# Optimization experiments

Measured on AMD Instinct MI355X. Metric: run time of the kernel, lower is better.

The kernel has to match this reference:

```python
import jax, jax.numpy as jnp
import numpy as np

B, T, HOR, N = 64, 12, 12, 1024
DIN, DOUT, YCOV, H, K, E = 1, 1, 1, 64, 3, 8


def setup_inputs() -> dict:
    key = jax.random.key(0)
    ks = jax.random.split(key, 10)
    def g(k, shape, s=1.0):
        return jax.random.normal(k, shape, dtype=jnp.float32) * s
    # xavier-ish scale for GCN weights: 1/sqrt(fan_in)
    gi = 1.0 / np.sqrt(K * (DIN + H))
    di = 1.0 / np.sqrt(K * (DOUT + YCOV + H))
    return {
        "x": jax.random.uniform(ks[0], (B, T, N, DIN), dtype=jnp.float32),
        "y_cov": jax.random.uniform(ks[1], (B, HOR, N, YCOV), dtype=jnp.float32),
        "node_emb": g(ks[2], (N, E), 1.0),
        "enc_gate_W": g(ks[3], (K * (DIN + H), 2 * H), gi),
        "enc_gate_b": jnp.zeros((2 * H,), jnp.float32),
        "enc_upd_W": g(ks[4], (K * (DIN + H), H), gi),
        "enc_upd_b": jnp.zeros((H,), jnp.float32),
        "dec_gate_W": g(ks[5], (K * (DOUT + YCOV + H), 2 * H), di),
        "dec_gate_b": jnp.zeros((2 * H,), jnp.float32),
        "dec_upd_W": g(ks[6], (K * (DOUT + YCOV + H), H), di),
        "dec_upd_b": jnp.zeros((H,), jnp.float32),
        "proj_W": g(ks[7], (H, DOUT), 1.0 / np.sqrt(H)),
        "proj_b": jnp.zeros((DOUT,), jnp.float32),
    }


def _cheb_supports(A):
    # support_set = [I, A, 2*A@A - I, ...], cheb_k terms
    s = [jnp.eye(A.shape[0], dtype=A.dtype), A]
    for _ in range(2, K):
        s.append(2.0 * A @ s[-1] - s[-2])
    return jnp.stack(s)  # [K, N, N]


def _gcn(x, sup, W, b):
    # x: [B,N,C]; sup: [K,N,N]; matches torch cat([s_k @ x], -1) ordering (k-major)
    bb, nn, cc = x.shape
    xg = jnp.einsum('knm,bmc->bnkc', sup, x).reshape(bb, nn, K * cc)
    return xg @ W + b


def _cell(x, h, sup, gW, gb, uW, ub):
    zr = jax.nn.sigmoid(_gcn(jnp.concatenate([x, h], -1), sup, gW, gb))
    z, r = jnp.split(zr, 2, axis=-1)
    hc = jnp.tanh(_gcn(jnp.concatenate([x, z * h], -1), sup, uW, ub))
    return r * h + (1.0 - r) * hc


def reference(x, y_cov, node_emb, enc_gate_W, enc_gate_b, enc_upd_W, enc_upd_b,
              dec_gate_W, dec_gate_b, dec_upd_W, dec_upd_b, proj_W, proj_b):
    # adaptive adjacency from node embeddings (AGCRN-style)
    A = jax.nn.softmax(jax.nn.relu(node_emb @ node_emb.T), axis=-1)
    sup = _cheb_supports(A)

    h0 = jnp.zeros((B, N, H), x.dtype)

    def enc_step(h, xt):
        h2 = _cell(xt, h, sup, enc_gate_W, enc_gate_b, enc_upd_W, enc_upd_b)
        return h2, None
    h_enc, _ = jax.lax.scan(enc_step, h0, jnp.swapaxes(x, 0, 1))  # final state [B,N,H]

    go0 = jnp.zeros((B, N, DOUT), x.dtype)

    def dec_step(carry, yt):
        h, go = carry
        h2 = _cell(jnp.concatenate([go, yt], -1), h, sup,
                   dec_gate_W, dec_gate_b, dec_upd_W, dec_upd_b)
        go2 = h2 @ proj_W + proj_b
        return (h2, go2), go2
    _, outs = jax.lax.scan(dec_step, (h_enc, go0), jnp.swapaxes(y_cov, 0, 1))
    return jnp.swapaxes(outs, 0, 1)  # [B, HOR, N, DOUT]
```

## Files before the change

kernel.cpp:

```cpp
#include <hip/hip_runtime.h>
#include <math.h>

constexpr int N = 1024, B = 64, T = 12, HOR = 12, H = 64, E = 8;
constexpr size_t NBH = 4194304;

constexpr size_t A_off   = 0;
constexpr size_t Pxy_off = 1048576;
constexpr size_t h_off   = Pxy_off + 3145728;
constexpr size_t Ph_off  = h_off + NBH;
constexpr size_t zh_off  = Ph_off + 2 * NBH;
constexpr size_t r_off   = zh_off + NBH;
constexpr size_t go_off  = r_off + NBH;
constexpr size_t A2_off  = go_off + 65536;
constexpr size_t Bth_off = A2_off + 1048576;
constexpr size_t Btz_off = Bth_off + 2162688;
constexpr size_t xyK_off = Btz_off + 2097152;
constexpr size_t Pgo_off = xyK_off + 786432;
constexpr size_t wp_off  = Pgo_off + 131072;

typedef __attribute__((ext_vector_type(8))) short short8;
typedef __attribute__((ext_vector_type(4))) float f32x4;

__device__ __forceinline__ unsigned f2bf(float x) {
  unsigned u = __float_as_uint(x);
  return (u + 0x7fffu + ((u >> 16) & 1u)) >> 16;
}
__device__ __forceinline__ float bf2f(unsigned h) {
  return __uint_as_float(h << 16);
}
__device__ __forceinline__ void split4(float4 v, uint2& hi, uint2& lo) {
  unsigned h0 = f2bf(v.x), h1 = f2bf(v.y), h2 = f2bf(v.z), h3 = f2bf(v.w);
  unsigned l0 = f2bf(v.x - bf2f(h0)), l1 = f2bf(v.y - bf2f(h1));
  unsigned l2 = f2bf(v.z - bf2f(h2)), l3 = f2bf(v.w - bf2f(h3));
  hi.x = (h0 & 0xffffu) | (h1 << 16); hi.y = (h2 & 0xffffu) | (h3 << 16);
  lo.x = (l0 & 0xffffu) | (l1 << 16); lo.y = (l2 & 0xffffu) | (l3 << 16);
}

typedef const __attribute__((address_space(1))) void gas_t;
typedef __attribute__((address_space(3))) void las_t;

__global__ __launch_bounds__(256) void build_A(const float* __restrict__ emb,
                                               float* __restrict__ A) {
  __shared__ float sE[N * E];
  __shared__ float sv[N];
  __shared__ float rmax[4], rsum[4];
  const int i = blockIdx.x;
  for (int idx = threadIdx.x; idx < N * E / 4; idx += 256)
    ((float4*)sE)[idx] = ((const float4*)emb)[idx];
  __syncthreads();
  float ei[E];
#pragma unroll
  for (int e = 0; e < E; ++e) ei[e] = sE[i * E + e];
  float mymax = 0.f;
  for (int j = threadIdx.x; j < N; j += 256) {
    float d = 0.f;
#pragma unroll
    for (int e = 0; e < E; ++e) d = fmaf(ei[e], sE[j * E + e], d);
    d = fmaxf(d, 0.f);
    sv[j] = d;
    mymax = fmaxf(mymax, d);
  }
  for (int off = 32; off; off >>= 1) mymax = fmaxf(mymax, __shfl_down(mymax, off));
  const int wid = threadIdx.x >> 6, lid = threadIdx.x & 63;
  if (lid == 0) rmax[wid] = mymax;
  __syncthreads();
  const float m = fmaxf(fmaxf(rmax[0], rmax[1]), fmaxf(rmax[2], rmax[3]));
  float mysum = 0.f;
  for (int j = threadIdx.x; j < N; j += 256) {
    float ev = expf(sv[j] - m);
    sv[j] = ev;
    mysum += ev;
  }
  for (int off = 32; off; off >>= 1) mysum += __shfl_down(mysum, off);
  if (lid == 0) rsum[wid] = mysum;
  __syncthreads();
  const float inv = 1.f / (rsum[0] + rsum[1] + rsum[2] + rsum[3]);
  for (int j = threadIdx.x; j < N; j += 256) A[i * N + j] = sv[j] * inv;
}

__global__ __launch_bounds__(256) void pack_split_S(const float* __restrict__ A,
                                                    ushort* __restrict__ L,
                                                    ushort* __restrict__ R) {
  __shared__ float tile[32][33];
  const int bx = blockIdx.x * 32;
  const int by = blockIdx.y * 32;
  const int tx = threadIdx.x & 31;
  const int tg = threadIdx.x >> 5;
#pragma unroll
  for (int p = 0; p < 4; ++p) {
    int ty = tg * 4 + p;
    tile[ty][tx] = A[(size_t)(by + ty) * 1024 + bx + tx];
  }
  __syncthreads();
#pragma unroll
  for (int p = 0; p < 4; ++p) {
    int ty = tg * 4 + p;
    float v = tile[ty][tx];
    unsigned h = f2bf(v);
    unsigned l = f2bf(v - bf2f(h));
    size_t lb = (size_t)(by + ty) * 3072 + 3 * (bx + tx);
    L[lb + 0] = (ushort)h; L[lb + 1] = (ushort)l; L[lb + 2] = (ushort)h;
    float w = tile[tx][ty];
    unsigned hh = f2bf(w);
    unsigned ll = f2bf(w - bf2f(hh));
    size_t rbi = (size_t)(bx + ty) * 3072 + 3 * (by + tx);
    R[rbi + 0] = (ushort)hh; R[rbi + 1] = (ushort)hh; R[rbi + 2] = (ushort)ll;
  }
}

__global__ __launch_bounds__(256) void conv_bf16(const float* __restrict__ src,
                                                 ushort* __restrict__ dst) {
  int i = blockIdx.x * 256 + threadIdx.x;
  float4 v = ((const float4*)src)[i];
  ushort4 o;
  o.x = (ushort)f2bf(v.x); o.y = (ushort)f2bf(v.y);
  o.z = (ushort)f2bf(v.z); o.w = (ushort)f2bf(v.w);
  ((ushort4*)dst)[i] = o;
}

__global__ __launch_bounds__(256) void conv_xyK(const float* __restrict__ src,
                                                ushort* __restrict__ dst, int off) {
  int id = blockIdx.x * 256 + threadIdx.x;
  int tb = id >> 10, n = id & 1023;
  int tt = tb >> 6, b = tb & 63;
  dst[(size_t)(off + tb) * 1024 + n] = (ushort)f2bf(src[((size_t)b * T + tt) * 1024 + n]);
}

__global__ __launch_bounds__(256) void pack_W(const float* __restrict__ W,
                                              ushort* __restrict__ out,
                                              int CIN, int NC, int xoff) {
  int idx = blockIdx.x * 256 + threadIdx.x;
  int total = 3 * 2 * NC * 32;
  if (idx >= total) return;
  int kk = idx & 31;
  int colrest = idx >> 5;
  int col = colrest % NC;
  int rest = colrest / NC;
  int half = rest & 1;
  int s = rest >> 1;
  float v = W[(size_t)(s * CIN + xoff + half * 32 + kk) * NC + col];
  unsigned hi = f2bf(v);
  unsigned lo = f2bf(v - bf2f(hi));
  size_t base = (size_t)((s * 2 + half) * 2) * NC * 32;
  out[base + (size_t)col * 32 + kk] = (ushort)hi;
  out[base + (size_t)NC * 32 + (size_t)col * 32 + kk] = (ushort)lo;
}

__global__ __launch_bounds__(256) void gemm_s2p(
    const ushort* __restrict__ L, const ushort* __restrict__ R,
    float* __restrict__ P) {
  __shared__ ushort As[128 * 32];
  __shared__ ushort Bs[128 * 32];
  const int t = threadIdx.x;
  const int wave = t >> 6, lane = t & 63;
  const int bm = blockIdx.y * 128, bn = blockIdx.x * 128;
  const int wm = (wave & 1) * 64, wn = (wave >> 1) * 64;
  float* Pz = P + (size_t)blockIdx.z * 1048576;
  const int kbase = blockIdx.z * 768;

  const ushort* aSrc[2]; const ushort* bSrc[2];
  ushort* aDst[2]; ushort* bDst[2];
#pragma unroll
  for (int u = 0; u < 2; ++u) {
    int idx = wave * 128 + u * 64 + lane;
    int row = idx >> 2;
    int kq = (idx & 3) * 8;
    aSrc[u] = L + (size_t)(bm + row) * 3072 + kq;
    bSrc[u] = R + (size_t)(bn + row) * 3072 + kq;
    aDst[u] = &As[(wave * 128 + u * 64) * 8];
    bDst[u] = &Bs[(wave * 128 + u * 64) * 8];
  }
  const int lr = lane & 15;
  const int lk = (lane >> 4) * 8;
  f32x4 acc[4][4];
#pragma unroll
  for (int i = 0; i < 4; ++i)
#pragma unroll
    for (int j = 0; j < 4; ++j) acc[i][j] = {0.f, 0.f, 0.f, 0.f};

  for (int k0 = kbase; k0 < kbase + 768; k0 += 32) {
#pragma unroll
    for (int u = 0; u < 2; ++u) {
      __builtin_amdgcn_global_load_lds((gas_t*)(aSrc[u] + k0), (las_t*)aDst[u], 16, 0, 0);
      __builtin_amdgcn_global_load_lds((gas_t*)(bSrc[u] + k0), (las_t*)bDst[u], 16, 0, 0);
    }
    __syncthreads();
    short8 a[4], b[4];
#pragma unroll
    for (int i = 0; i < 4; ++i) a[i] = *(const short8*)&As[(wm + i * 16 + lr) * 32 + lk];
#pragma unroll
    for (int j = 0; j < 4; ++j) b[j] = *(const short8*)&Bs[(wn + j * 16 + lr) * 32 + lk];
#pragma unroll
    for (int i = 0; i < 4; ++i)
#pragma unroll
      for (int j = 0; j < 4; ++j)
        acc[i][j] = __builtin_amdgcn_mfma_f32_16x16x32_bf16(a[i], b[j], acc[i][j], 0, 0, 0);
    __syncthreads();
  }
  const int cr = (lane >> 4) * 4;
  const int cc = lane & 15;
#pragma unroll
  for (int i = 0; i < 4; ++i)
#pragma unroll
    for (int j = 0; j < 4; ++j) {
      int gm = bm + wm + i * 16 + cr;
      int gn = bn + wn + j * 16 + cc;
#pragma unroll
      for (int r = 0; r < 4; ++r)
        Pz[(size_t)(gm + r) * 1024 + gn] = acc[i][j][r];
    }
}

__global__ __launch_bounds__(256) void comb_s2(const float* __restrict__ P,
                                               ushort* __restrict__ A2) {
  int idx = blockIdx.x * 256 + threadIdx.x;
  float4 a = ((const float4*)P)[idx];
  float4 b = ((const float4*)(P + 1048576))[idx];
  float4 c = ((const float4*)(P + 2097152))[idx];
  float4 d = ((const float4*)(P + 3145728))[idx];
  int base = idx << 2;
  int m = base >> 10, c0 = base & 1023;
  float v0 = 2.f * (a.x + b.x + c.x + d.x) - (m == c0 + 0 ? 1.f : 0.f);
  float v1 = 2.f * (a.y + b.y + c.y + d.y) - (m == c0 + 1 ? 1.f : 0.f);
  float v2 = 2.f * (a.z + b.z + c.z + d.z) - (m == c0 + 2 ? 1.f : 0.f);
  float v3 = 2.f * (a.w + b.w + c.w + d.w) - (m == c0 + 3 ? 1.f : 0.f);
  ushort4 o;
  o.x = (ushort)f2bf(v0); o.y = (ushort)f2bf(v1);
  o.z = (ushort)f2bf(v2); o.w = (ushort)f2bf(v3);
  ((ushort4*)(A2 + 1048576))[idx] = o;
}

template <int CMODE>
__global__ __launch_bounds__(256) void gemm_bt(
    const ushort* __restrict__ A2, const ushort* __restrict__ Bt, int n1,
    float* __restrict__ C1, float* __restrict__ C2) {
  __shared__ ushort As[2][128 * 32];
  __shared__ ushort Bs[2][128 * 32];
  const int t = threadIdx.x;
  const int wave = t >> 6, lane = t & 63;
  const int bm = blockIdx.y * 128, bn = blockIdx.x * 128;
  const int wm = (wave & 1) * 64, wn = (wave >> 1) * 64;

  const ushort* aSrc[2]; const ushort* bSrc[2];
  ushort* aDst[2][2]; ushort* bDst[2][2];
#pragma unroll
  for (int u = 0; u < 2; ++u) {
    int idx = wave * 128 + u * 64 + lane;
    int row = idx >> 2;
    int kq = (idx & 3) * 8;
    aSrc[u] = A2 + (size_t)(bm + row) * 1024 + kq;
    bSrc[u] = Bt + (size_t)(bn + row) * 1024 + kq;
#pragma unroll
    for (int p = 0; p < 2; ++p) {
      aDst[p][u] = &As[p][(wave * 128 + u * 64) * 8];
      bDst[p][u] = &Bs[p][(wave * 128 + u * 64) * 8];
    }
  }
  const int lr = lane & 15, lk = (lane >> 4) * 8;
  int aOff[4], bOff[4];
#pragma unroll
  for (int i = 0; i < 4; ++i) {
    aOff[i] = (wm + i * 16 + lr) * 32 + lk;
    bOff[i] = (wn + i * 16 + lr) * 32 + lk;
  }
  f32x4 acc[4][4];
#pragma unroll
  for (int i = 0; i < 4; ++i)
#pragma unroll
    for (int j = 0; j < 4; ++j) acc[i][j] = {0.f, 0.f, 0.f, 0.f};

  for (int k0 = 0; k0 < 1024; k0 += 64) {
#pragma unroll
    for (int p = 0; p < 2; ++p)
#pragma unroll
      for (int u = 0; u < 2; ++u) {
        __builtin_amdgcn_global_load_lds((gas_t*)(aSrc[u] + k0 + p * 32),
                                         (las_t*)aDst[p][u], 16, 0, 0);
        __builtin_amdgcn_global_load_lds((gas_t*)(bSrc[u] + k0 + p * 32),
                                         (las_t*)bDst[p][u], 16, 0, 0);
      }
    __syncthreads();
#pragma unroll
    for (int p = 0; p < 2; ++p) {
      short8 a[4], b[4];
#pragma unroll
      for (int i = 0; i < 4; ++i) a[i] = *(const short8*)&As[p][aOff[i]];
#pragma unroll
      for (int j = 0; j < 4; ++j) b[j] = *(const short8*)&Bs[p][bOff[j]];
#pragma unroll
      for (int i = 0; i < 4; ++i)
#pragma unroll
        for (int j = 0; j < 4; ++j)
          acc[i][j] = __builtin_amdgcn_mfma_f32_16x16x32_bf16(a[i], b[j], acc[i][j], 0, 0, 0);
    }
    __syncthreads();
  }

  const int cr = (lane >> 4) * 4;
  const int cc = lane & 15;
#pragma unroll
  for (int i = 0; i < 4; ++i) {
#pragma unroll
    for (int j = 0; j < 4; ++j) {
      int gm = bm + wm + i * 16 + cr;
      int gn = bn + wn + j * 16 + cc;
      if (gn < n1) {
        if (CMODE == 0) {
          float* p = C1 + (size_t)gm * n1 + gn;
#pragma unroll
          for (int r = 0; r < 4; ++r) p[(size_t)r * n1] = acc[i][j][r];
        } else {
          int half = gm >> 10, nn = gm & 1023;
          float* p = C1 + (size_t)half * NBH +
                     ((size_t)(gn >> 6) * 1024 + nn) * 64 + (gn & 63);
#pragma unroll
          for (int r = 0; r < 4; ++r) p[(size_t)r * 64] = acc[i][j][r];
        }
      } else if (C2 != nullptr && gn < n1 + 64) {
        float* p = C2 + (size_t)gm * 64 + (gn - n1);
#pragma unroll
        for (int r = 0; r < 4; ++r) p[(size_t)r * 64] = acc[i][j][r];
      }
    }
  }
}

template <int NX>
__global__ __launch_bounds__(256) void gate_mfma(
    const float* __restrict__ hmat, const float* __restrict__ Ph,
    const ushort* __restrict__ Wp, const float* __restrict__ Wf, const float* __restrict__ bias,
    const float* __restrict__ xb0, int xbs0, const float* __restrict__ xp0, int xs0,
    const float* __restrict__ xb1, int xbs1, const float* __restrict__ xp1, int xs1,
    float* __restrict__ zh, float* __restrict__ rbuf, ushort* __restrict__ Btz) {
  constexpr int CIN = NX + 64;
  __shared__ ushort Ah[128 * 32], Al[128 * 32];
  __shared__ ushort Bh[128 * 32], Bl[128 * 32];
  __shared__ ushort transT[64 * 136];
  __shared__ float sxv[3][2][128];
  __shared__ float sWx[3][2][128];
  const int t = threadIdx.x;
  const int wave = t >> 6, lane = t & 63;
  const int bm = blockIdx.x * 128;
  const int wm = (wave & 1) * 64, wn = (wave >> 1) * 64;
  const int lr = lane & 15, lk = (lane >> 4) * 8;
  const float* s1 = Ph;
  const float* s2 = Ph + NBH;

  if (t < 128) {
    int grow = bm + t;
    int n = grow & 1023, b = grow >> 10;
    sxv[0][0][t] = xb0[(size_t)b * xbs0 + n];
    sxv[1][0][t] = xp0[(size_t)n * xs0 + b];
    sxv[2][0][t] = xp0[(size_t)1024 * xs0 + (size_t)n * xs0 + b];
    if (NX == 2) {
      sxv[0][1][t] = xb1[(size_t)b * xbs1 + n];
      sxv[1][1][t] = xp1[(size_t)n * xs1 + b];
      sxv[2][1][t] = xp1[(size_t)1024 * xs1 + (size_t)n * xs1 + b];
    }
  } else {
    int col = t - 128;
#pragma unroll
    for (int s = 0; s < 3; ++s)
#pragma unroll
      for (int f = 0; f < NX; ++f)
        sWx[s][f][col] = Wf[(size_t)(s * CIN + f) * 128 + col];
  }

  f32x4 acc[4][4];
#pragma unroll
  for (int i = 0; i < 4; ++i)
#pragma unroll
    for (int j = 0; j < 4; ++j) acc[i][j] = {0.f, 0.f, 0.f, 0.f};

  for (int it = 0; it < 6; ++it) {
    const int s = it >> 1, half = it & 1, j0 = half * 32;
    const float* src = (s == 0) ? hmat : ((s == 1) ? s1 : s2);
#pragma unroll
    for (int p = 0; p < 4; ++p) {
      int f = p * 256 + t;
      int row = f >> 3;
      int jq = (f & 7) * 4;
      float4 v = *(const float4*)(src + (size_t)(bm + row) * 64 + j0 + jq);
      uint2 hi, lo;
      split4(v, hi, lo);
      *(uint2*)&Ah[row * 32 + jq] = hi;
      *(uint2*)&Al[row * 32 + jq] = lo;
    }
    const ushort* wph = Wp + (size_t)((s * 2 + half) * 2) * (128 * 32);
    const ushort* wpl = wph + 128 * 32;
#pragma unroll
    for (int u = 0; u < 2; ++u) {
      int idx = wave * 128 + u * 64 + lane;
      __builtin_amdgcn_global_load_lds((gas_t*)(wph + idx * 8), (las_t*)&Bh[idx * 8], 16, 0, 0);
      __builtin_amdgcn_global_load_lds((gas_t*)(wpl + idx * 8), (las_t*)&Bl[idx * 8], 16, 0, 0);
    }
    __syncthreads();
    short8 ah[4], al[4], bh[4], bl[4];
#pragma unroll
    for (int i = 0; i < 4; ++i) {
      ah[i] = *(const short8*)&Ah[(wm + i * 16 + lr) * 32 + lk];
      al[i] = *(const short8*)&Al[(wm + i * 16 + lr) * 32 + lk];
    }
#pragma unroll
    for (int j = 0; j < 4; ++j) {
      bh[j] = *(const short8*)&Bh[(wn + j * 16 + lr) * 32 + lk];
      bl[j] = *(const short8*)&Bl[(wn + j * 16 + lr) * 32 + lk];
    }
#pragma unroll
    for (int i = 0; i < 4; ++i)
#pragma unroll
      for (int j = 0; j < 4; ++j) {
        acc[i][j] = __builtin_amdgcn_mfma_f32_16x16x32_bf16(ah[i], bh[j], acc[i][j], 0, 0, 0);
        acc[i][j] = __builtin_amdgcn_mfma_f32_16x16x32_bf16(al[i], bh[j], acc[i][j], 0, 0, 0);
        acc[i][j] = __builtin_amdgcn_mfma_f32_16x16x32_bf16(ah[i], bl[j], acc[i][j], 0, 0, 0);
      }
    __syncthreads();
  }

  const int cr = (lane >> 4) * 4;
  const int cc = lane & 15;
#pragma unroll
  for (int i = 0; i < 4; ++i) {
#pragma unroll
    for (int j = 0; j < 4; ++j) {
      int col = wn + j * 16 + cc;
      float bcol = bias[col];
#pragma unroll
      for (int r = 0; r < 4; ++r) {
        int rowl = wm + i * 16 + cr + r;
        int grow = bm + rowl;
        float v = acc[i][j][r] + bcol;
#pragma unroll
        for (int s = 0; s < 3; ++s)
#pragma unroll
          for (int f = 0; f < NX; ++f)
            v = fmaf(sxv[s][f][rowl], sWx[s][f][col], v);
        float sig = 1.f / (1.f + expf(-v));
        if (col < 64) {
          float zv = sig * hmat[(size_t)grow * 64 + col];
          zh[(size_t)grow * 64 + col] = zv;
          transT[col * 136 + rowl] = (ushort)f2bf(zv);
        } else {
          rbuf[(size_t)grow * 64 + col - 64] = sig;
        }
      }
    }
  }
  __syncthreads();
  const int bq = bm >> 10, nb = bm & 1023;
  for (int idx = t; idx < 1024; idx += 256) {
    int j = idx >> 4, ch = idx & 15;
    uint4 v = *(const uint4*)&transT[j * 136 + ch * 8];
    *(uint4*)(Btz + (((size_t)(bq * 64 + j)) << 10) + nb + ch * 8) = v;
  }
}

template <int NX, int PROJ>
__global__ __launch_bounds__(256) void upd_mfma(
    float* __restrict__ hmat, const float* __restrict__ zhb, const float* __restrict__ Pzh,
    const ushort* __restrict__ Wp, const float* __restrict__ Wf, const float* __restrict__ bias,
    const float* __restrict__ xb0, int xbs0, const float* __restrict__ xp0, int xs0,
    const float* __restrict__ xb1, int xbs1, const float* __restrict__ xp1, int xs1,
    const float* __restrict__ rbuf, ushort* __restrict__ Bth,
    const float* __restrict__ pW, const float* __restrict__ pb,
    float* __restrict__ gobuf, float* __restrict__ outp, int tstep) {
  constexpr int CIN = NX + 64;
  __shared__ ushort Ah[128 * 32], Al[128 * 32];
  __shared__ ushort Bh[64 * 32], Bl[64 * 32];
  __shared__ ushort transT[64 * 136];
  __shared__ float sxv[3][2][128];
  __shared__ float sWx[3][2][64];
  __shared__ float part[2][128];
  const int t = threadIdx.x;
  const int wave = t >> 6, lane = t & 63;
  const int bm = blockIdx.x * 128;
  const int wm = (wave & 1) * 64, wn = (wave >> 1) * 32;
  const int lr = lane & 15, lk = (lane >> 4) * 8;
  const float* s1 = Pzh;
  const float* s2 = Pzh + NBH;

  if (t < 128) {
    int grow = bm + t;
    int n = grow & 1023, b = grow >> 10;
    sxv[0][0][t] = xb0[(size_t)b * xbs0 + n];
    sxv[1][0][t] = xp0[(size_t)n * xs0 + b];
    sxv[2][0][t] = xp0[(size_t)1024 * xs0 + (size_t)n * xs0 + b];
    if (NX == 2) {
      sxv[0][1][t] = xb1[(size_t)b * xbs1 + n];
      sxv[1][1][t] = xp1[(size_t)n * xs1 + b];
      sxv[2][1][t] = xp1[(size_t)1024 * xs1 + (size_t)n * xs1 + b];
    }
  } else if (t < 192) {
    int col = t - 128;
#pragma unroll
    for (int s = 0; s < 3; ++s)
#pragma unroll
      for (int f = 0; f < NX; ++f)
        sWx[s][f][col] = Wf[(size_t)(s * CIN + f) * 64 + col];
  }

  f32x4 acc[4][2];
#pragma unroll
  for (int i = 0; i < 4; ++i)
#pragma unroll
    for (int j = 0; j < 2; ++j) acc[i][j] = {0.f, 0.f, 0.f, 0.f};

  for (int it = 0; it < 6; ++it) {
    const int s = it >> 1, half = it & 1, j0 = half * 32;
    const float* src = (s == 0) ? zhb : ((s == 1) ? s1 : s2);
#pragma unroll
    for (int p = 0; p < 4; ++p) {
      int f = p * 256 + t;
      int row = f >> 3;
      int jq = (f & 7) * 4;
      float4 v = *(const float4*)(src + (size_t)(bm + row) * 64 + j0 + jq);
      uint2 hi, lo;
      split4(v, hi, lo);
      *(uint2*)&Ah[row * 32 + jq] = hi;
      *(uint2*)&Al[row * 32 + jq] = lo;
    }
    const ushort* wph = Wp + (size_t)((s * 2 + half) * 2) * (64 * 32);
    const ushort* wpl = wph + 64 * 32;
    {
      int idx = wave * 64 + lane;
      __builtin_amdgcn_global_load_lds((gas_t*)(wph + idx * 8), (las_t*)&Bh[idx * 8], 16, 0, 0);
      __builtin_amdgcn_global_load_lds((gas_t*)(wpl + idx * 8), (las_t*)&Bl[idx * 8], 16, 0, 0);
    }
    __syncthreads();
    short8 ah[4], al[4], bh[2], bl[2];
#pragma unroll
    for (int i = 0; i < 4; ++i) {
      ah[i] = *(const short8*)&Ah[(wm + i * 16 + lr) * 32 + lk];
      al[i] = *(const short8*)&Al[(wm + i * 16 + lr) * 32 + lk];
    }
#pragma unroll
    for (int j = 0; j < 2; ++j) {
      bh[j] = *(const short8*)&Bh[(wn + j * 16 + lr) * 32 + lk];
      bl[j] = *(const short8*)&Bl[(wn + j * 16 + lr) * 32 + lk];
    }
#pragma unroll
    for (int i = 0; i < 4; ++i)
#pragma unroll
      for (int j = 0; j < 2; ++j) {
        acc[i][j] = __builtin_amdgcn_mfma_f32_16x16x32_bf16(ah[i], bh[j], acc[i][j], 0, 0, 0);
        acc[i][j] = __builtin_amdgcn_mfma_f32_16x16x32_bf16(al[i], bh[j], acc[i][j], 0, 0, 0);
        acc[i][j] = __builtin_amdgcn_mfma_f32_16x16x32_bf16(ah[i], bl[j], acc[i][j], 0, 0, 0);
      }
    __syncthreads();
  }

  const int cr = (lane >> 4) * 4;
  const int cc = lane & 15;
  float psv[4][4];
#pragma unroll
  for (int i = 0; i < 4; ++i)
#pragma unroll
    for (int r = 0; r < 4; ++r) psv[i][r] = 0.f;

#pragma unroll
  for (int i = 0; i < 4; ++i) {
#pragma unroll
    for (int j = 0; j < 2; ++j) {
      int col = wn + j * 16 + cc;
      float bcol = bias[col];
      float pwc = PROJ ? pW[col] : 0.f;
#pragma unroll
      for (int r = 0; r < 4; ++r) {
        int rowl = wm + i * 16 + cr + r;
        int grow = bm + rowl;
        float v = acc[i][j][r] + bcol;
#pragma unroll
        for (int s = 0; s < 3; ++s)
#pragma unroll
          for (int f = 0; f < NX; ++f)
            v = fmaf(sxv[s][f][rowl], sWx[s][f][col], v);
        float hc = tanhf(v);
        size_t idx = (size_t)grow * 64 + col;
        float rr = rbuf[idx];
        float ho = hmat[idx];
        float o = rr * ho + (1.f - rr) * hc;
        hmat[idx] = o;
        transT[col * 136 + rowl] = (ushort)f2bf(o);
        if (PROJ) psv[i][r] += o * pwc;
      }
    }
  }
  if (PROJ) {
#pragma unroll
    for (int i = 0; i < 4; ++i)
#pragma unroll
      for (int r = 0; r < 4; ++r)
#pragma unroll
        for (int off = 8; off; off >>= 1)
          psv[i][r] += __shfl_down(psv[i][r], off, 16);
    if (cc == 0) {
#pragma unroll
      for (int i = 0; i < 4; ++i)
#pragma unroll
        for (int r = 0; r < 4; ++r)
          part[wn >> 5][wm + i * 16 + cr + r] = psv[i][r];
    }
  }
  __syncthreads();
  const int bq = bm >> 10, nb = bm & 1023;
  for (int idx = t; idx < 1024; idx += 256) {
    int j = idx >> 4, ch = idx & 15;
    uint4 v = *(const uint4*)&transT[j * 136 + ch * 8];
    *(uint4*)(Bth + (((size_t)(bq * 64 + j)) << 10) + nb + ch * 8) = v;
  }
  if (PROJ && t < 128) {
    int grow = bm + t;
    int n = grow & 1023, b = grow >> 10;
    float g = part[0][t] + part[1][t] + pb[0];
    gobuf[grow] = g;
    outp[((size_t)b * HOR + tstep) * N + n] = g;
    Bth[((size_t)(4096 + b)) * 1024 + n] = (ushort)f2bf(g);
  }
}

extern "C" void kernel_launch(void* const* d_in, const int* in_sizes, int n_in,
                              void* d_out, int out_size, void* d_ws, size_t ws_size,
                              hipStream_t stream) {
  const float* x    = (const float*)d_in[0];
  const float* ycov = (const float*)d_in[1];
  const float* emb  = (const float*)d_in[2];
  const float* egW  = (const float*)d_in[3];
  const float* egb  = (const float*)d_in[4];
  const float* euW  = (const float*)d_in[5];
  const float* eub  = (const float*)d_in[6];
  const float* dgW  = (const float*)d_in[7];
  const float* dgb  = (const float*)d_in[8];
  const float* duW  = (const float*)d_in[9];
  const float* dub  = (const float*)d_in[10];
  const float* pW   = (const float*)d_in[11];
  const float* pb   = (const float*)d_in[12];
  float* out = (float*)d_out;
  float* ws  = (float*)d_ws;

  float* Amat = ws + A_off;
  float* Pxy  = ws + Pxy_off;
  float* hmat = ws + h_off;
  float* Ph   = ws + Ph_off;
  float* zh   = ws + zh_off;
  float* rb   = ws + r_off;
  float* gob  = ws + go_off;
  float* Pgo  = ws + Pgo_off;
  ushort* A2   = (ushort*)(ws + A2_off);
  ushort* Bth  = (ushort*)(ws + Bth_off);
  ushort* Btz  = (ushort*)(ws + Btz_off);
  ushort* xyK  = (ushort*)(ws + xyK_off);
  ushort* AspL = (ushort*)(ws + zh_off);
  ushort* AspR = (ushort*)(ws + r_off);
  float*  Pp   = ws + Ph_off;
  ushort* WPge = (ushort*)(ws + wp_off);
  ushort* WPgd = WPge + 2 * 24576;
  ushort* WPue = WPgd + 2 * 24576;
  ushort* WPud = WPue + 2 * 12288;

  build_A<<<N, 256, 0, stream>>>(emb, Amat);
  pack_split_S<<<dim3(32, 32), 256, 0, stream>>>(Amat, AspL, AspR);
  gemm_s2p<<<dim3(8, 8, 4), 256, 0, stream>>>(AspL, AspR, Pp);
  comb_s2<<<1024, 256, 0, stream>>>(Pp, A2);
  conv_bf16<<<1024, 256, 0, stream>>>(Amat, A2);
  conv_xyK<<<3072, 256, 0, stream>>>(x, xyK, 0);
  conv_xyK<<<3072, 256, 0, stream>>>(ycov, xyK, 768);
  pack_W<<<(3 * 2 * 128 * 32 + 255) / 256, 256, 0, stream>>>(egW, WPge, 65, 128, 1);
  pack_W<<<(3 * 2 * 128 * 32 + 255) / 256, 256, 0, stream>>>(dgW, WPgd, 66, 128, 2);
  pack_W<<<(3 * 2 * 64 * 32 + 255) / 256, 256, 0, stream>>>(euW, WPue, 65, 64, 1);
  pack_W<<<(3 * 2 * 64 * 32 + 255) / 256, 256, 0, stream>>>(duW, WPud, 66, 64, 2);
  gemm_bt<0><<<dim3(12, 16), 256, 0, stream>>>(A2, xyK, 1536, Pxy, nullptr);
  (void)hipMemsetAsync(hmat, 0, NBH * sizeof(float), stream);
  (void)hipMemsetAsync(Ph, 0, 2 * NBH * sizeof(float), stream);
  (void)hipMemsetAsync(gob, 0, 65536 * sizeof(float), stream);
  (void)hipMemsetAsync(Bth + (size_t)4096 * 1024, 0, 128 * 1024 * sizeof(ushort), stream);

  for (int t = 0; t < T; ++t) {
    if (t > 0)
      gemm_bt<1><<<dim3(32, 16), 256, 0, stream>>>(A2, Bth, 4096, Ph, nullptr);
    gate_mfma<1><<<512, 256, 0, stream>>>(hmat, Ph, WPge, egW, egb,
                                          x + t * 1024, T * 1024, Pxy + t * 64, 1536,
                                          nullptr, 0, nullptr, 0, zh, rb, Btz);
    if (t > 0)
      gemm_bt<1><<<dim3(32, 16), 256, 0, stream>>>(A2, Btz, 4096, Ph, nullptr);
    upd_mfma<1, 0><<<512, 256, 0, stream>>>(hmat, zh, Ph, WPue, euW, eub,
                                            x + t * 1024, T * 1024, Pxy + t * 64, 1536,
                                            nullptr, 0, nullptr, 0, rb, Bth,
                                            nullptr, nullptr, nullptr, nullptr, 0);
  }

  for (int t = 0; t < HOR; ++t) {
    gemm_bt<1><<<dim3(33, 16), 256, 0, stream>>>(A2, Bth, 4096, Ph, Pgo);
    gate_mfma<2><<<512, 256, 0, stream>>>(hmat, Ph, WPgd, dgW, dgb,
                                          gob, 1024, Pgo, 64,
                                          ycov + t * 1024, HOR * 1024,
                                          Pxy + 768 + t * 64, 1536, zh, rb, Btz);
    gemm_bt<1><<<dim3(32, 16), 256, 0, stream>>>(A2, Btz, 4096, Ph, nullptr);
    upd_mfma<2, 1><<<512, 256, 0, stream>>>(hmat, zh, Ph, WPud, duW, dub,
                                            gob, 1024, Pgo, 64,
                                            ycov + t * 1024, HOR * 1024,
                                            Pxy + 768 + t * 64, 1536,
                                            rb, Bth, pW, pb, gob, out, t);
  }
}
```

Baseline: 3.089 ms.

## Halve row tile in gate/update MFMA kernels, alias LDS, prefetch A tiles

The gate and update MFMA kernels now process 64 rows per block instead of 128, so twice as many blocks launch. The LDS buffers are merged into one array, with the transpose staging area reusing the A/B space, and launch bounds ask for 4 blocks per CU. A register prefetch of the next A-slice's fp32 data is issued after the barrier so the global load overlaps the MFMA work. The goal is more parallelism and occupancy across the 256 CUs and hidden load latency; the cost is that each block reloads the weight tiles twice as often relative to the rows it computes.

```diff
diff --git a/kernel.cpp b/kernel.cpp
--- a/kernel.cpp
+++ b/kernel.cpp
@@ -326,27 +326,29 @@
 }
 
 template <int NX>
-__global__ __launch_bounds__(256) void gate_mfma(
+__global__ __launch_bounds__(256, 4) void gate_mfma(
     const float* __restrict__ hmat, const float* __restrict__ Ph,
     const ushort* __restrict__ Wp, const float* __restrict__ Wf, const float* __restrict__ bias,
     const float* __restrict__ xb0, int xbs0, const float* __restrict__ xp0, int xs0,
     const float* __restrict__ xb1, int xbs1, const float* __restrict__ xp1, int xs1,
     float* __restrict__ zh, float* __restrict__ rbuf, ushort* __restrict__ Btz) {
   constexpr int CIN = NX + 64;
-  __shared__ ushort Ah[128 * 32], Al[128 * 32];
-  __shared__ ushort Bh[128 * 32], Bl[128 * 32];
-  __shared__ ushort transT[64 * 136];
-  __shared__ float sxv[3][2][128];
+  __shared__ ushort smem[12288];
+  ushort* Ah = smem;
+  ushort* Al = smem + 2048;
+  ushort* Bh = smem + 4096;
+  ushort* Bl = smem + 8192;
+  ushort* transT = smem;
+  __shared__ float sxv[3][2][64];
   __shared__ float sWx[3][2][128];
   const int t = threadIdx.x;
   const int wave = t >> 6, lane = t & 63;
-  const int bm = blockIdx.x * 128;
-  const int wm = (wave & 1) * 64, wn = (wave >> 1) * 64;
+  const int bm = blockIdx.x * 64;
+  const int wm = (wave & 1) * 32, wn = (wave >> 1) * 64;
   const int lr = lane & 15, lk = (lane >> 4) * 8;
-  const float* s1 = Ph;
-  const float* s2 = Ph + NBH;
-
-  if (t < 128) {
+  const float* srcs[3] = {hmat, Ph, Ph + NBH};
+
+  if (t < 64) {
     int grow = bm + t;
     int n = grow & 1023, b = grow >> 10;
     sxv[0][0][t] = xb0[(size_t)b * xbs0 + n];
@@ -357,8 +359,8 @@
       sxv[1][1][t] = xp1[(size_t)n * xs1 + b];
       sxv[2][1][t] = xp1[(size_t)1024 * xs1 + (size_t)n * xs1 + b];
     }
-  } else {
-    int col = t - 128;
+  } else if (t < 192) {
+    int col = t - 64;
 #pragma unroll
     for (int s = 0; s < 3; ++s)
 #pragma unroll
@@ -366,25 +368,32 @@
         sWx[s][f][col] = Wf[(size_t)(s * CIN + f) * 128 + col];
   }
 
-  f32x4 acc[4][4];
-#pragma unroll
-  for (int i = 0; i < 4; ++i)
+  int arow[2], ajq[2];
+#pragma unroll
+  for (int p = 0; p < 2; ++p) {
+    int f = p * 256 + t;
+    arow[p] = f >> 3;
+    ajq[p] = (f & 7) * 4;
+  }
+  float4 pf[2];
+#pragma unroll
+  for (int p = 0; p < 2; ++p)
+    pf[p] = *(const float4*)(hmat + (size_t)(bm + arow[p]) * 64 + ajq[p]);
+
+  f32x4 acc[2][4];
+#pragma unroll
+  for (int i = 0; i < 2; ++i)
 #pragma unroll
     for (int j = 0; j < 4; ++j) acc[i][j] = {0.f, 0.f, 0.f, 0.f};
 
   for (int it = 0; it < 6; ++it) {
-    const int s = it >> 1, half = it & 1, j0 = half * 32;
-    const float* src = (s == 0) ? hmat : ((s == 1) ? s1 : s2);
-#pragma unroll
-    for (int p = 0; p < 4; ++p) {
-      int f = p * 256 + t;
-      int row = f >> 3;
-      int jq = (f & 7) * 4;
-      float4 v = *(const float4*)(src + (size_t)(bm + row) * 64 + j0 + jq);
+    const int s = it >> 1, half = it & 1;
+#pragma unroll
+    for (int p = 0; p < 2; ++p) {
       uint2 hi, lo;
-      split4(v, hi, lo);
-      *(uint2*)&Ah[row * 32 + jq] = hi;
-      *(uint2*)&Al[row * 32 + jq] = lo;
+      split4(pf[p], hi, lo);
+      *(uint2*)&Ah[arow[p] * 32 + ajq[p]] = hi;
+      *(uint2*)&Al[arow[p] * 32 + ajq[p]] = lo;
     }
     const ushort* wph = Wp + (size_t)((s * 2 + half) * 2) * (128 * 32);
     const ushort* wpl = wph + 128 * 32;
@@ -395,9 +404,16 @@
       __builtin_amdgcn_global_load_lds((gas_t*)(wpl + idx * 8), (las_t*)&Bl[idx * 8], 16, 0, 0);
     }
     __syncthreads();
-    short8 ah[4], al[4], bh[4], bl[4];
-#pragma unroll
-    for (int i = 0; i < 4; ++i) {
+    if (it < 5) {
+      const float* nsrc = srcs[(it + 1) >> 1];
+      const int nj0 = ((it + 1) & 1) * 32;
+#pragma unroll
+      for (int p = 0; p < 2; ++p)
+        pf[p] = *(const float4*)(nsrc + (size_t)(bm + arow[p]) * 64 + nj0 + ajq[p]);
+    }
+    short8 ah[2], al[2], bh[4], bl[4];
+#pragma unroll
+    for (int i = 0; i < 2; ++i) {
       ah[i] = *(const short8*)&Ah[(wm + i * 16 + lr) * 32 + lk];
       al[i] = *(const short8*)&Al[(wm + i * 16 + lr) * 32 + lk];
     }
@@ -407,7 +423,7 @@
       bl[j] = *(const short8*)&Bl[(wn + j * 16 + lr) * 32 + lk];
     }
 #pragma unroll
-    for (int i = 0; i < 4; ++i)
+    for (int i = 0; i < 2; ++i)
 #pragma unroll
       for (int j = 0; j < 4; ++j) {
         acc[i][j] = __builtin_amdgcn_mfma_f32_16x16x32_bf16(ah[i], bh[j], acc[i][j], 0, 0, 0);
@@ -420,7 +436,7 @@
   const int cr = (lane >> 4) * 4;
   const int cc = lane & 15;
 #pragma unroll
-  for (int i = 0; i < 4; ++i) {
+  for (int i = 0; i < 2; ++i) {
 #pragma unroll
     for (int j = 0; j < 4; ++j) {
       int col = wn + j * 16 + cc;
@@ -439,7 +455,7 @@
         if (col < 64) {
           float zv = sig * hmat[(size_t)grow * 64 + col];
           zh[(size_t)grow * 64 + col] = zv;
-          transT[col * 136 + rowl] = (ushort)f2bf(zv);
+          transT[col * 72 + rowl] = (ushort)f2bf(zv);
         } else {
           rbuf[(size_t)grow * 64 + col - 64] = sig;
         }
@@ -448,15 +464,15 @@
   }
   __syncthreads();
   const int bq = bm >> 10, nb = bm & 1023;
-  for (int idx = t; idx < 1024; idx += 256) {
-    int j = idx >> 4, ch = idx & 15;
-    uint4 v = *(const uint4*)&transT[j * 136 + ch * 8];
+  for (int idx = t; idx < 512; idx += 256) {
+    int j = idx >> 3, ch = idx & 7;
+    uint4 v = *(const uint4*)&transT[j * 72 + ch * 8];
     *(uint4*)(Btz + (((size_t)(bq * 64 + j)) << 10) + nb + ch * 8) = v;
   }
 }
 
 template <int NX, int PROJ>
-__global__ __launch_bounds__(256) void upd_mfma(
+__global__ __launch_bounds__(256, 4) void upd_mfma(
     float* __restrict__ hmat, const float* __restrict__ zhb, const float* __restrict__ Pzh,
     const ushort* __restrict__ Wp, const float* __restrict__ Wf, const float* __restrict__ bias,
     const float* __restrict__ xb0, int xbs0, const float* __restrict__ xp0, int xs0,
@@ -465,21 +481,23 @@
     const float* __restrict__ pW, const float* __restrict__ pb,
     float* __restrict__ gobuf, float* __restrict__ outp, int tstep) {
   constexpr int CIN = NX + 64;
-  __shared__ ushort Ah[128 * 32], Al[128 * 32];
-  __shared__ ushort Bh[64 * 32], Bl[64 * 32];
-  __shared__ ushort transT[64 * 136];
-  __shared__ float sxv[3][2][128];
+  __shared__ ushort smem[8192];
+  ushort* Ah = smem;
+  ushort* Al = smem + 2048;
+  ushort* Bh = smem + 4096;
+  ushort* Bl = smem + 6144;
+  ushort* transT = smem;
+  __shared__ float sxv[3][2][64];
   __shared__ float sWx[3][2][64];
-  __shared__ float part[2][128];
+  __shared__ float part[2][64];
   const int t = threadIdx.x;
   const int wave = t >> 6, lane = t & 63;
-  const int bm = blockIdx.x * 128;
-  const int wm = (wave & 1) * 64, wn = (wave >> 1) * 32;
+  const int bm = blockIdx.x * 64;
+  const int wm = (wave & 1) * 32, wn = (wave >> 1) * 32;
   const int lr = lane & 15, lk = (lane >> 4) * 8;
-  const float* s1 = Pzh;
-  const float* s2 = Pzh + NBH;
-
-  if (t < 128) {
+  const float* srcs[3] = {zhb, Pzh, Pzh + NBH};
+
+  if (t < 64) {
     int grow = bm + t;
     int n = grow & 1023, b = grow >> 10;
     sxv[0][0][t] = xb0[(size_t)b * xbs0 + n];
@@ -490,8 +508,8 @@
       sxv[1][1][t] = xp1[(size_t)n * xs1 + b];
       sxv[2][1][t] = xp1[(size_t)1024 * xs1 + (size_t)n * xs1 + b];
     }
-  } else if (t < 192) {
-    int col = t - 128;
+  } else if (t < 128) {
+    int col = t - 64;
 #pragma unroll
     for (int s = 0; s < 3; ++s)
 #pragma unroll
@@ -499,25 +517,32 @@
         sWx[s][f][col] = Wf[(size_t)(s * CIN + f) * 64 + col];
   }
 
-  f32x4 acc[4][2];
-#pragma unroll
-  for (int i = 0; i < 4; ++i)
+  int arow[2], ajq[2];
+#pragma unroll
+  for (int p = 0; p < 2; ++p) {
+    int f = p * 256 + t;
+    arow[p] = f >> 3;
+    ajq[p] = (f & 7) * 4;
+  }
+  float4 pf[2];
+#pragma unroll
+  for (int p = 0; p < 2; ++p)
+    pf[p] = *(const float4*)(zhb + (size_t)(bm + arow[p]) * 64 + ajq[p]);
+
+  f32x4 acc[2][2];
+#pragma unroll
+  for (int i = 0; i < 2; ++i)
 #pragma unroll
     for (int j = 0; j < 2; ++j) acc[i][j] = {0.f, 0.f, 0.f, 0.f};
 
   for (int it = 0; it < 6; ++it) {
-    const int s = it >> 1, half = it & 1, j0 = half * 32;
-    const float* src = (s == 0) ? zhb : ((s == 1) ? s1 : s2);
-#pragma unroll
-    for (int p = 0; p < 4; ++p) {
-      int f = p * 256 + t;
-      int row = f >> 3;
-      int jq = (f & 7) * 4;
-      float4 v = *(const float4*)(src + (size_t)(bm + row) * 64 + j0 + jq);
+    const int s = it >> 1, half = it & 1;
+#pragma unroll
+    for (int p = 0; p < 2; ++p) {
       uint2 hi, lo;
-      split4(v, hi, lo);
-      *(uint2*)&Ah[row * 32 + jq] = hi;
-      *(uint2*)&Al[row * 32 + jq] = lo;
+      split4(pf[p], hi, lo);
+      *(uint2*)&Ah[arow[p] * 32 + ajq[p]] = hi;
+      *(uint2*)&Al[arow[p] * 32 + ajq[p]] = lo;
     }
     const ushort* wph = Wp + (size_t)((s * 2 + half) * 2) * (64 * 32);
     const ushort* wpl = wph + 64 * 32;
@@ -527,9 +552,16 @@
       __builtin_amdgcn_global_load_lds((gas_t*)(wpl + idx * 8), (las_t*)&Bl[idx * 8], 16, 0, 0);
     }
     __syncthreads();
-    short8 ah[4], al[4], bh[2], bl[2];
-#pragma unroll
-    for (int i = 0; i < 4; ++i) {
+    if (it < 5) {
+      const float* nsrc = srcs[(it + 1) >> 1];
+      const int nj0 = ((it + 1) & 1) * 32;
+#pragma unroll
+      for (int p = 0; p < 2; ++p)
+        pf[p] = *(const float4*)(nsrc + (size_t)(bm + arow[p]) * 64 + nj0 + ajq[p]);
+    }
+    short8 ah[2], al[2], bh[2], bl[2];
+#pragma unroll
+    for (int i = 0; i < 2; ++i) {
       ah[i] = *(const short8*)&Ah[(wm + i * 16 + lr) * 32 + lk];
       al[i] = *(const short8*)&Al[(wm + i * 16 + lr) * 32 + lk];
     }
@@ -539,7 +571,7 @@
       bl[j] = *(const short8*)&Bl[(wn + j * 16 + lr) * 32 + lk];
     }
 #pragma unroll
-    for (int i = 0; i < 4; ++i)
+    for (int i = 0; i < 2; ++i)
 #pragma unroll
       for (int j = 0; j < 2; ++j) {
         acc[i][j] = __builtin_amdgcn_mfma_f32_16x16x32_bf16(ah[i], bh[j], acc[i][j], 0, 0, 0);
@@ -551,14 +583,14 @@
 
   const int cr = (lane >> 4) * 4;
   const int cc = lane & 15;
-  float psv[4][4];
-#pragma unroll
-  for (int i = 0; i < 4; ++i)
+  float psv[2][4];
+#pragma unroll
+  for (int i = 0; i < 2; ++i)
 #pragma unroll
     for (int r = 0; r < 4; ++r) psv[i][r] = 0.f;
 
 #pragma unroll
-  for (int i = 0; i < 4; ++i) {
+  for (int i = 0; i < 2; ++i) {
 #pragma unroll
     for (int j = 0; j < 2; ++j) {
       int col = wn + j * 16 + cc;
@@ -580,14 +612,14 @@
         float ho = hmat[idx];
         float o = rr * ho + (1.f - rr) * hc;
         hmat[idx] = o;
-        transT[col * 136 + rowl] = (ushort)f2bf(o);
+        transT[col * 72 + rowl] = (ushort)f2bf(o);
         if (PROJ) psv[i][r] += o * pwc;
       }
     }
   }
   if (PROJ) {
 #pragma unroll
-    for (int i = 0; i < 4; ++i)
+    for (int i = 0; i < 2; ++i)
 #pragma unroll
       for (int r = 0; r < 4; ++r)
 #pragma unroll
@@ -595,7 +627,7 @@
           psv[i][r] += __shfl_down(psv[i][r], off, 16);
     if (cc == 0) {
 #pragma unroll
-      for (int i = 0; i < 4; ++i)
+      for (int i = 0; i < 2; ++i)
 #pragma unroll
         for (int r = 0; r < 4; ++r)
           part[wn >> 5][wm + i * 16 + cr + r] = psv[i][r];
@@ -603,12 +635,12 @@
   }
   __syncthreads();
   const int bq = bm >> 10, nb = bm & 1023;
-  for (int idx = t; idx < 1024; idx += 256) {
-    int j = idx >> 4, ch = idx & 15;
-    uint4 v = *(const uint4*)&transT[j * 136 + ch * 8];
+  for (int idx = t; idx < 512; idx += 256) {
+    int j = idx >> 3, ch = idx & 7;
+    uint4 v = *(const uint4*)&transT[j * 72 + ch * 8];
     *(uint4*)(Bth + (((size_t)(bq * 64 + j)) << 10) + nb + ch * 8) = v;
   }
-  if (PROJ && t < 128) {
+  if (PROJ && t < 64) {
     int grow = bm + t;
     int n = grow & 1023, b = grow >> 10;
     float g = part[0][t] + part[1][t] + pb[0];
@@ -677,28 +709,28 @@
   for (int t = 0; t < T; ++t) {
     if (t > 0)
       gemm_bt<1><<<dim3(32, 16), 256, 0, stream>>>(A2, Bth, 4096, Ph, nullptr);
-    gate_mfma<1><<<512, 256, 0, stream>>>(hmat, Ph, WPge, egW, egb,
-                                          x + t * 1024, T * 1024, Pxy + t * 64, 1536,
-                                          nullptr, 0, nullptr, 0, zh, rb, Btz);
+    gate_mfma<1><<<1024, 256, 0, stream>>>(hmat, Ph, WPge, egW, egb,
+                                           x + t * 1024, T * 1024, Pxy + t * 64, 1536,
+                                           nullptr, 0, nullptr, 0, zh, rb, Btz);
     if (t > 0)
       gemm_bt<1><<<dim3(32, 16), 256, 0, stream>>>(A2, Btz, 4096, Ph, nullptr);
-    upd_mfma<1, 0><<<512, 256, 0, stream>>>(hmat, zh, Ph, WPue, euW, eub,
-                                            x + t * 1024, T * 1024, Pxy + t * 64, 1536,
-                                            nullptr, 0, nullptr, 0, rb, Bth,
-                                            nullptr, nullptr, nullptr, nullptr, 0);
+    upd_mfma<1, 0><<<1024, 256, 0, stream>>>(hmat, zh, Ph, WPue, euW, eub,
+                                             x + t * 1024, T * 1024, Pxy + t * 64, 1536,
+                                             nullptr, 0, nullptr, 0, rb, Bth,
+                                             nullptr, nullptr, nullptr, nullptr, 0);
   }
 
   for (int t = 0; t < HOR; ++t) {
     gemm_bt<1><<<dim3(33, 16), 256, 0, stream>>>(A2, Bth, 4096, Ph, Pgo);
-    gate_mfma<2><<<512, 256, 0, stream>>>(hmat, Ph, WPgd, dgW, dgb,
-                                          gob, 1024, Pgo, 64,
-                                          ycov + t * 1024, HOR * 1024,
-                                          Pxy + 768 + t * 64, 1536, zh, rb, Btz);
+    gate_mfma<2><<<1024, 256, 0, stream>>>(hmat, Ph, WPgd, dgW, dgb,
+                                           gob, 1024, Pgo, 64,
+                                           ycov + t * 1024, HOR * 1024,
+                                           Pxy + 768 + t * 64, 1536, zh, rb, Btz);
     gemm_bt<1><<<dim3(32, 16), 256, 0, stream>>>(A2, Btz, 4096, Ph, nullptr);
-    upd_mfma<2, 1><<<512, 256, 0, stream>>>(hmat, zh, Ph, WPud, duW, dub,
-                                            gob, 1024, Pgo, 64,
-                                            ycov + t * 1024, HOR * 1024,
-                                            Pxy + 768 + t * 64, 1536,
-                                            rb, Bth, pW, pb, gob, out, t);
-  }
-}
+    upd_mfma<2, 1><<<1024, 256, 0, stream>>>(hmat, zh, Ph, WPud, duW, dub,
+                                             gob, 1024, Pgo, 64,
+                                             ycov + t * 1024, HOR * 1024,
+                                             Pxy + 768 + t * 64, 1536,
+                                             rb, Bth, pW, pb, gob, out, t);
+  }
+}
```

After: 2.701 ms. -12.5%, faster.
